# Performance work log

Measured on AMD Instinct MI355X. Metric: run time of the kernel, lower is better.

## Reference

```python
import jax, jax.numpy as jnp
import numpy as np

Nknn = 10
Np = 20
N = 524288
DOWN, LEFT, RIGHT, UP, WIDTH = -5.0, -5.0, 5.0, 5.0, 1.0


def setup_inputs() -> dict:
    key = jax.random.key(0)
    ks = jax.random.split(key, 20)
    def p(k, shape, fan_in):
        return jax.random.normal(k, shape, jnp.float32) / jnp.sqrt(jnp.float32(fan_in))
    inp = {
        "t": jax.random.uniform(ks[0], (1,), jnp.float32),
        "y": jax.random.normal(ks[1], (N, 4 + 2 * Np), jnp.float32),
        # net1: Linear(4,8) -> ReLU -> Linear(8,2)
        "w1a": p(ks[2], (4, 8), 4),   "b1a": p(ks[3], (8,), 4),
        "w1b": p(ks[4], (8, 2), 8),   "b1b": p(ks[5], (2,), 8),
        # net2: Linear(1,16) -> ReLU -> Linear(16,8) -> ReLU -> Linear(8,1)
        "w2a": p(ks[6], (1, 16), 1),  "b2a": p(ks[7], (16,), 1),
        "w2b": p(ks[8], (16, 8), 16), "b2b": p(ks[9], (8,), 16),
        "w2c": p(ks[10], (8, 1), 8),  "b2c": p(ks[11], (1,), 8),
        # net3: same architecture as net2
        "w3a": p(ks[12], (1, 16), 1), "b3a": p(ks[13], (16,), 1),
        "w3b": p(ks[14], (16, 8), 16),"b3b": p(ks[15], (8,), 16),
        "w3c": p(ks[16], (8, 1), 8),  "b3c": p(ks[17], (1,), 8),
    }
    return inp


def _mlp3(x, wa, ba, wb, bb, wc, bc):
    # Linear -> ReLU -> Linear -> ReLU -> Linear, applied on last axis
    h = jax.nn.relu(x @ wa + ba)
    h = jax.nn.relu(h @ wb + bb)
    return h @ wc + bc


def reference(t, y, w1a, b1a, w1b, b1b, w2a, b2a, w2b, b2b, w2c, b2c,
              w3a, b3a, w3b, b3b, w3c, b3c):
    y = y.astype(jnp.float32)
    theX = y[:, 0:2]            # positions [N,2]
    theV = y[:, 2:4]            # velocities [N,2]
    ux = y[:, 4:4 + 2 * Nknn].reshape(-1, Nknn, 2)  # neighbor offsets [N,Nknn,2]

    dxdt = theV

    # goal-attraction term f1
    door = jnp.array([RIGHT + 0.6, 0.0], jnp.float32)
    diff = door - theX
    unit_e = diff / jnp.sqrt(jnp.sum(diff * diff, axis=1, keepdims=True))
    h = jax.nn.relu(jnp.concatenate([unit_e, theV], axis=1) @ w1a + b1a)
    f1 = h @ w1b + b1b          # [N,2]

    # wall-repulsion term f2; rows inside the door gap get rightdist=100
    x0 = theX[:, 0:1]
    x1 = theX[:, 1:2]
    rightdist = jnp.where((x1 < WIDTH) & (x1 > -WIDTH), 100.0, RIGHT - x0)
    wall_in = jnp.stack([x0 - LEFT, x1 - DOWN, UP - x1, rightdist], axis=1)  # [N,4,1]
    o = _mlp3(wall_in, w2a, b2a, w2b, bb=b2b, wc=w2c, bc=b2c) if False else _mlp3(wall_in, w2a, b2a, w2b, b2b, w2c, b2c)  # [N,4,1]
    # directions: [1,0], [0,1], [0,-1], [-1,0]
    f2 = jnp.concatenate([o[:, 0] - o[:, 3], o[:, 1] - o[:, 2]], axis=1)  # [N,2]

    # neighbor-repulsion term f3 (vectorized over Nknn)
    d = jnp.sqrt(jnp.sum(ux * ux, axis=2, keepdims=True))  # [N,Nknn,1]
    f3 = -jnp.sum(_mlp3(d, w3a, b3a, w3b, b3b, w3c, b3c) * ux / d, axis=1)  # [N,2]

    dvdt = (f1 + f2 + f3) / 80.0
    dudt = jnp.zeros((y.shape[0], 2 * Nknn), y.dtype)
    result = jnp.concatenate([dxdt, dvdt, dudt], axis=1)  # [N, 4 + 2*Nknn]

    # zero out agents that have exited (x > RIGHT)
    result = jnp.where((theX[:, 0] > RIGHT)[:, None], 0.0, result)
    return result
```

## Files before the change

### kernel.cpp

```cpp
#include <hip/hip_runtime.h>

#define NROW  524288
#define BLK   256
#define TPB   2
#define NKNN  10
#define YCOLS 44
#define OCOLS 24

#define TBL    128
#define T2_LO  (-2.0f)
#define T3_LO  (0.0f)
#define T_H    (1.0f / 8.0f)
#define T_INVH 8.0f
#define SROW   25

typedef float f32x4 __attribute__((ext_vector_type(4)));

__device__ __forceinline__ float mlp_scalar_g(float s,
    const float* __restrict__ wa, const float* __restrict__ ba,
    const float* __restrict__ wb, const float* __restrict__ bb,
    const float* __restrict__ wc, const float* __restrict__ bc) {
    float h[16];
#pragma unroll
    for (int j = 0; j < 16; ++j)
        h[j] = fmaxf(fmaf(s, wa[j], ba[j]), 0.0f);
    float g[8];
#pragma unroll
    for (int k = 0; k < 8; ++k) g[k] = bb[k];
#pragma unroll
    for (int j = 0; j < 16; ++j) {
        float hj = h[j];
#pragma unroll
        for (int k = 0; k < 8; ++k)
            g[k] = fmaf(hj, wb[j * 8 + k], g[k]);
    }
    float o = bc[0];
#pragma unroll
    for (int k = 0; k < 8; ++k)
        o = fmaf(fmaxf(g[k], 0.0f), wc[k], o);
    return o;
}

__device__ __forceinline__ float tbl_eval(const float* __restrict__ T, float s, float lo) {
    float u = (s - lo) * T_INVH;
    u = fminf(fmaxf(u, 0.0f), (float)TBL - 1.001f);
    int i = (int)u;
    float f = u - (float)i;
    float va = T[i];
    float vb = T[i + 1];
    return fmaf(f, vb - va, va);
}

__device__ __forceinline__ void load_tile(const f32x4* __restrict__ yb,
                                          int w, int lane, f32x4 ld[6]) {
#pragma unroll
    for (int i = 0; i < 6; ++i) {
        int j  = lane + i * 64;
        int rr = j / 6;
        int cc = j - rr * 6;
        ld[i]  = yb[(64 * w + rr) * 11 + cc];
    }
}

__device__ __forceinline__ void stage_tile(float* __restrict__ Sf,
                                           int w, int lane, const f32x4 ld[6]) {
#pragma unroll
    for (int i = 0; i < 6; ++i) {
        int j  = lane + i * 64;
        int rr = j / 6;
        int cc = j - rr * 6;
        int base = (64 * w + rr) * SROW + 4 * cc;
        Sf[base + 0] = ld[i].x;
        Sf[base + 1] = ld[i].y;
        Sf[base + 2] = ld[i].z;
        Sf[base + 3] = ld[i].w;
    }
}

__device__ __forceinline__ void compute_row(float* __restrict__ Sf, int t,
    const float* __restrict__ T2v, const float* __restrict__ T3v, float o100,
    const float* __restrict__ w1a, const float* __restrict__ b1a,
    const float* __restrict__ w1b, const float* __restrict__ b1b)
{
    float* R = Sf + t * SROW;
    float x0 = R[0], x1 = R[1], vx = R[2], vy = R[3];
    float us[2 * NKNN];
#pragma unroll
    for (int m = 0; m < 2 * NKNN; ++m)
        us[m] = R[4 + m];

    float dx = 5.6f - x0;
    float dy = 0.0f - x1;
    float inv = rsqrtf(fmaf(dx, dx, dy * dy));
    float in1[4] = { dx * inv, dy * inv, vx, vy };
    float h1[8];
#pragma unroll
    for (int j = 0; j < 8; ++j) {
        float s = b1a[j];
#pragma unroll
        for (int k = 0; k < 4; ++k)
            s = fmaf(in1[k], w1a[k * 8 + j], s);
        h1[j] = fmaxf(s, 0.0f);
    }
    float f1x = b1b[0];
    float f1y = b1b[1];
#pragma unroll
    for (int j = 0; j < 8; ++j) {
        f1x = fmaf(h1[j], w1b[j * 2 + 0], f1x);
        f1y = fmaf(h1[j], w1b[j * 2 + 1], f1y);
    }

    bool corridor = (x1 < 1.0f) && (x1 > -1.0f);
    float o0 = tbl_eval(T2v, x0 + 5.0f, T2_LO);
    float o1 = tbl_eval(T2v, x1 + 5.0f, T2_LO);
    float o2 = tbl_eval(T2v, 5.0f - x1, T2_LO);
    float o3 = corridor ? o100 : tbl_eval(T2v, 5.0f - x0, T2_LO);
    float f2x = o0 - o3;
    float f2y = o1 - o2;

    float f3x = 0.0f, f3y = 0.0f;
#pragma unroll
    for (int n = 0; n < NKNN; ++n) {
        float uxn = us[2 * n + 0];
        float uyn = us[2 * n + 1];
        float s2  = fmaf(uxn, uxn, uyn * uyn);
        float idn = rsqrtf(s2);
        float d   = s2 * idn;
        float m   = tbl_eval(T3v, d, T3_LO);
        float c   = m * idn;
        f3x = fmaf(-c, uxn, f3x);
        f3y = fmaf(-c, uyn, f3y);
    }

    bool dead = (x0 > 5.0f);
    const float k80 = 1.0f / 80.0f;
    R[0] = dead ? 0.0f : vx;
    R[1] = dead ? 0.0f : vy;
    R[2] = dead ? 0.0f : (f1x + f2x + f3x) * k80;
    R[3] = dead ? 0.0f : (f1y + f2y + f3y) * k80;
}

__device__ __forceinline__ void store_tile(f32x4* __restrict__ ob,
                                           const float* __restrict__ Sf,
                                           int w, int lane) {
#pragma unroll
    for (int i = 0; i < 6; ++i) {
        int j  = lane + i * 64;
        int rr = j / 6;
        int cc = j - rr * 6;
        f32x4 v = (f32x4)(0.0f);
        if (cc == 0) {
            const float* R = Sf + (64 * w + rr) * SROW;
            v.x = R[0]; v.y = R[1]; v.z = R[2]; v.w = R[3];
        }
        __builtin_nontemporal_store(v, &ob[384 * w + j]);
    }
}

__global__ __launch_bounds__(BLK) void odefunc_kernel(
    const float* __restrict__ y,
    const float* __restrict__ w1a, const float* __restrict__ b1a,
    const float* __restrict__ w1b, const float* __restrict__ b1b,
    const float* __restrict__ w2a, const float* __restrict__ b2a,
    const float* __restrict__ w2b, const float* __restrict__ b2b,
    const float* __restrict__ w2c, const float* __restrict__ b2c,
    const float* __restrict__ w3a, const float* __restrict__ b3a,
    const float* __restrict__ w3b, const float* __restrict__ b3b,
    const float* __restrict__ w3c, const float* __restrict__ b3c,
    float* __restrict__ out)
{
    __shared__ float Sf[BLK * SROW];
    __shared__ float T2v[TBL];
    __shared__ float T3v[TBL];
    __shared__ float o100s;

    const int t    = threadIdx.x;
    const int w    = t >> 6;
    const int lane = t & 63;

    const f32x4* yb0 = reinterpret_cast<const f32x4*>(y)
                     + (size_t)blockIdx.x * TPB * BLK * (YCOLS / 4);
    const f32x4* yb1 = yb0 + BLK * (YCOLS / 4);
    f32x4* ob0 = reinterpret_cast<f32x4*>(out)
               + (size_t)blockIdx.x * TPB * BLK * (OCOLS / 4);
    f32x4* ob1 = ob0 + BLK * (OCOLS / 4);

    f32x4 ld0[6];
    load_tile(yb0, w, lane, ld0);

    if (t < TBL) {
        T2v[t] = mlp_scalar_g(T2_LO + (float)t * T_H, w2a, b2a, w2b, b2b, w2c, b2c);
        if (t == 0)
            o100s = mlp_scalar_g(100.0f, w2a, b2a, w2b, b2b, w2c, b2c);
    } else {
        int i3 = t - TBL;
        T3v[i3] = mlp_scalar_g(T3_LO + (float)i3 * T_H, w3a, b3a, w3b, b3b, w3c, b3c);
    }

    __syncthreads();
    const float o100 = o100s;

    stage_tile(Sf, w, lane, ld0);
    __builtin_amdgcn_wave_barrier();

    f32x4 ld1[6];
    load_tile(yb1, w, lane, ld1);

    compute_row(Sf, t, T2v, T3v, o100, w1a, b1a, w1b, b1b);
    __builtin_amdgcn_wave_barrier();
    store_tile(ob0, Sf, w, lane);
    __builtin_amdgcn_wave_barrier();

    stage_tile(Sf, w, lane, ld1);
    __builtin_amdgcn_wave_barrier();

    compute_row(Sf, t, T2v, T3v, o100, w1a, b1a, w1b, b1b);
    __builtin_amdgcn_wave_barrier();
    store_tile(ob1, Sf, w, lane);
}

extern "C" void kernel_launch(void* const* d_in, const int* in_sizes, int n_in,
                              void* d_out, int out_size, void* d_ws, size_t ws_size,
                              hipStream_t stream) {
    int iy = 1;
    for (int i = 0; i < n_in; ++i) {
        if (in_sizes[i] == NROW * YCOLS) { iy = i; break; }
    }
    const float* y   = (const float*)d_in[iy];
    const float* w1a = (const float*)d_in[iy + 1];
    const float* b1a = (const float*)d_in[iy + 2];
    const float* w1b = (const float*)d_in[iy + 3];
    const float* b1b = (const float*)d_in[iy + 4];
    const float* w2a = (const float*)d_in[iy + 5];
    const float* b2a = (const float*)d_in[iy + 6];
    const float* w2b = (const float*)d_in[iy + 7];
    const float* b2b = (const float*)d_in[iy + 8];
    const float* w2c = (const float*)d_in[iy + 9];
    const float* b2c = (const float*)d_in[iy + 10];
    const float* w3a = (const float*)d_in[iy + 11];
    const float* b3a = (const float*)d_in[iy + 12];
    const float* w3b = (const float*)d_in[iy + 13];
    const float* b3b = (const float*)d_in[iy + 14];
    const float* w3c = (const float*)d_in[iy + 15];
    const float* b3c = (const float*)d_in[iy + 16];
    float* out = (float*)d_out;

    hipLaunchKernelGGL(odefunc_kernel, dim3(NROW / (BLK * TPB)), dim3(BLK), 0, stream,
                       y, w1a, b1a, w1b, b1b,
                       w2a, b2a, w2b, b2b, w2c, b2c,
                       w3a, b3a, w3b, b3b, w3c, b3c, out);
}
```

Measured before the change: 25.90 us.

## Process one tile per block and stage rows in two LDS halves

The kernel goes from two 256-row tiles per block to one, doubling the grid. Each row is now staged through LDS in two passes: columns 0-11 first, then columns 12-23, with the stride reduced from 25 to 13 floats. The goal is to shrink LDS per block to raise occupancy and to overlap the second-half staging with the f1/f2 compute. The cost is that every block rebuilds its lookup tables, so twice as many blocks repeat that setup work.

```diff
diff --git a/kernel.cpp b/kernel.cpp
--- a/kernel.cpp
+++ b/kernel.cpp
@@ -2,7 +2,6 @@
 
 #define NROW  524288
 #define BLK   256
-#define TPB   2
 #define NKNN  10
 #define YCOLS 44
 #define OCOLS 24
@@ -12,7 +11,7 @@
 #define T3_LO  (0.0f)
 #define T_H    (1.0f / 8.0f)
 #define T_INVH 8.0f
-#define SROW   25
+#define SROW   13
 
 typedef float f32x4 __attribute__((ext_vector_type(4)));
 
@@ -49,112 +48,6 @@
     float va = T[i];
     float vb = T[i + 1];
     return fmaf(f, vb - va, va);
-}
-
-__device__ __forceinline__ void load_tile(const f32x4* __restrict__ yb,
-                                          int w, int lane, f32x4 ld[6]) {
-#pragma unroll
-    for (int i = 0; i < 6; ++i) {
-        int j  = lane + i * 64;
-        int rr = j / 6;
-        int cc = j - rr * 6;
-        ld[i]  = yb[(64 * w + rr) * 11 + cc];
-    }
-}
-
-__device__ __forceinline__ void stage_tile(float* __restrict__ Sf,
-                                           int w, int lane, const f32x4 ld[6]) {
-#pragma unroll
-    for (int i = 0; i < 6; ++i) {
-        int j  = lane + i * 64;
-        int rr = j / 6;
-        int cc = j - rr * 6;
-        int base = (64 * w + rr) * SROW + 4 * cc;
-        Sf[base + 0] = ld[i].x;
-        Sf[base + 1] = ld[i].y;
-        Sf[base + 2] = ld[i].z;
-        Sf[base + 3] = ld[i].w;
-    }
-}
-
-__device__ __forceinline__ void compute_row(float* __restrict__ Sf, int t,
-    const float* __restrict__ T2v, const float* __restrict__ T3v, float o100,
-    const float* __restrict__ w1a, const float* __restrict__ b1a,
-    const float* __restrict__ w1b, const float* __restrict__ b1b)
-{
-    float* R = Sf + t * SROW;
-    float x0 = R[0], x1 = R[1], vx = R[2], vy = R[3];
-    float us[2 * NKNN];
-#pragma unroll
-    for (int m = 0; m < 2 * NKNN; ++m)
-        us[m] = R[4 + m];
-
-    float dx = 5.6f - x0;
-    float dy = 0.0f - x1;
-    float inv = rsqrtf(fmaf(dx, dx, dy * dy));
-    float in1[4] = { dx * inv, dy * inv, vx, vy };
-    float h1[8];
-#pragma unroll
-    for (int j = 0; j < 8; ++j) {
-        float s = b1a[j];
-#pragma unroll
-        for (int k = 0; k < 4; ++k)
-            s = fmaf(in1[k], w1a[k * 8 + j], s);
-        h1[j] = fmaxf(s, 0.0f);
-    }
-    float f1x = b1b[0];
-    float f1y = b1b[1];
-#pragma unroll
-    for (int j = 0; j < 8; ++j) {
-        f1x = fmaf(h1[j], w1b[j * 2 + 0], f1x);
-        f1y = fmaf(h1[j], w1b[j * 2 + 1], f1y);
-    }
-
-    bool corridor = (x1 < 1.0f) && (x1 > -1.0f);
-    float o0 = tbl_eval(T2v, x0 + 5.0f, T2_LO);
-    float o1 = tbl_eval(T2v, x1 + 5.0f, T2_LO);
-    float o2 = tbl_eval(T2v, 5.0f - x1, T2_LO);
-    float o3 = corridor ? o100 : tbl_eval(T2v, 5.0f - x0, T2_LO);
-    float f2x = o0 - o3;
-    float f2y = o1 - o2;
-
-    float f3x = 0.0f, f3y = 0.0f;
-#pragma unroll
-    for (int n = 0; n < NKNN; ++n) {
-        float uxn = us[2 * n + 0];
-        float uyn = us[2 * n + 1];
-        float s2  = fmaf(uxn, uxn, uyn * uyn);
-        float idn = rsqrtf(s2);
-        float d   = s2 * idn;
-        float m   = tbl_eval(T3v, d, T3_LO);
-        float c   = m * idn;
-        f3x = fmaf(-c, uxn, f3x);
-        f3y = fmaf(-c, uyn, f3y);
-    }
-
-    bool dead = (x0 > 5.0f);
-    const float k80 = 1.0f / 80.0f;
-    R[0] = dead ? 0.0f : vx;
-    R[1] = dead ? 0.0f : vy;
-    R[2] = dead ? 0.0f : (f1x + f2x + f3x) * k80;
-    R[3] = dead ? 0.0f : (f1y + f2y + f3y) * k80;
-}
-
-__device__ __forceinline__ void store_tile(f32x4* __restrict__ ob,
-                                           const float* __restrict__ Sf,
-                                           int w, int lane) {
-#pragma unroll
-    for (int i = 0; i < 6; ++i) {
-        int j  = lane + i * 64;
-        int rr = j / 6;
-        int cc = j - rr * 6;
-        f32x4 v = (f32x4)(0.0f);
-        if (cc == 0) {
-            const float* R = Sf + (64 * w + rr) * SROW;
-            v.x = R[0]; v.y = R[1]; v.z = R[2]; v.w = R[3];
-        }
-        __builtin_nontemporal_store(v, &ob[384 * w + j]);
-    }
 }
 
 __global__ __launch_bounds__(BLK) void odefunc_kernel(
@@ -178,15 +71,29 @@
     const int w    = t >> 6;
     const int lane = t & 63;
 
-    const f32x4* yb0 = reinterpret_cast<const f32x4*>(y)
-                     + (size_t)blockIdx.x * TPB * BLK * (YCOLS / 4);
-    const f32x4* yb1 = yb0 + BLK * (YCOLS / 4);
-    f32x4* ob0 = reinterpret_cast<f32x4*>(out)
-               + (size_t)blockIdx.x * TPB * BLK * (OCOLS / 4);
-    f32x4* ob1 = ob0 + BLK * (OCOLS / 4);
-
-    f32x4 ld0[6];
-    load_tile(yb0, w, lane, ld0);
+    const f32x4* yb = reinterpret_cast<const f32x4*>(y)
+                    + (size_t)blockIdx.x * BLK * (YCOLS / 4);
+    f32x4* ob = reinterpret_cast<f32x4*>(out)
+              + (size_t)blockIdx.x * BLK * (OCOLS / 4);
+
+    f32x4 ldA[3], ldB[3];
+    int rrA[3], ccA[3], rrB[3], ccB[3];
+#pragma unroll
+    for (int i = 0; i < 3; ++i) {
+        int j  = lane + i * 64;
+        int rr = j / 3;
+        int cc = j - rr * 3;
+        rrA[i] = rr; ccA[i] = cc;
+        ldA[i] = yb[(64 * w + rr) * 11 + cc];
+    }
+#pragma unroll
+    for (int i = 0; i < 3; ++i) {
+        int j  = lane + i * 64;
+        int rr = j / 3;
+        int cc = j - rr * 3;
+        rrB[i] = rr; ccB[i] = cc;
+        ldB[i] = yb[(64 * w + rr) * 11 + (cc + 3)];
+    }
 
     if (t < TBL) {
         T2v[t] = mlp_scalar_g(T2_LO + (float)t * T_H, w2a, b2a, w2b, b2b, w2c, b2c);
@@ -200,23 +107,114 @@
     __syncthreads();
     const float o100 = o100s;
 
-    stage_tile(Sf, w, lane, ld0);
-    __builtin_amdgcn_wave_barrier();
-
-    f32x4 ld1[6];
-    load_tile(yb1, w, lane, ld1);
-
-    compute_row(Sf, t, T2v, T3v, o100, w1a, b1a, w1b, b1b);
-    __builtin_amdgcn_wave_barrier();
-    store_tile(ob0, Sf, w, lane);
-    __builtin_amdgcn_wave_barrier();
-
-    stage_tile(Sf, w, lane, ld1);
-    __builtin_amdgcn_wave_barrier();
-
-    compute_row(Sf, t, T2v, T3v, o100, w1a, b1a, w1b, b1b);
-    __builtin_amdgcn_wave_barrier();
-    store_tile(ob1, Sf, w, lane);
+#pragma unroll
+    for (int i = 0; i < 3; ++i) {
+        int base = (64 * w + rrA[i]) * SROW + 4 * ccA[i];
+        Sf[base + 0] = ldA[i].x;
+        Sf[base + 1] = ldA[i].y;
+        Sf[base + 2] = ldA[i].z;
+        Sf[base + 3] = ldA[i].w;
+    }
+    __builtin_amdgcn_wave_barrier();
+
+    float* R = Sf + t * SROW;
+    float x0 = R[0], x1 = R[1], vx = R[2], vy = R[3];
+    float uA[8];
+#pragma unroll
+    for (int m = 0; m < 8; ++m) uA[m] = R[4 + m];
+    __builtin_amdgcn_wave_barrier();
+
+    float dxm = 5.6f - x0;
+    float dym = 0.0f - x1;
+    float inv = rsqrtf(fmaf(dxm, dxm, dym * dym));
+    float in1[4] = { dxm * inv, dym * inv, vx, vy };
+    float h1[8];
+#pragma unroll
+    for (int j = 0; j < 8; ++j) {
+        float s = b1a[j];
+#pragma unroll
+        for (int k = 0; k < 4; ++k)
+            s = fmaf(in1[k], w1a[k * 8 + j], s);
+        h1[j] = fmaxf(s, 0.0f);
+    }
+    float f1x = b1b[0];
+    float f1y = b1b[1];
+#pragma unroll
+    for (int j = 0; j < 8; ++j) {
+        f1x = fmaf(h1[j], w1b[j * 2 + 0], f1x);
+        f1y = fmaf(h1[j], w1b[j * 2 + 1], f1y);
+    }
+
+    bool corridor = (x1 < 1.0f) && (x1 > -1.0f);
+    float o0 = tbl_eval(T2v, x0 + 5.0f, T2_LO);
+    float o1 = tbl_eval(T2v, x1 + 5.0f, T2_LO);
+    float o2 = tbl_eval(T2v, 5.0f - x1, T2_LO);
+    float o3 = corridor ? o100 : tbl_eval(T2v, 5.0f - x0, T2_LO);
+    float f2x = o0 - o3;
+    float f2y = o1 - o2;
+
+    float f3x = 0.0f, f3y = 0.0f;
+#pragma unroll
+    for (int n = 0; n < 4; ++n) {
+        float uxn = uA[2 * n + 0];
+        float uyn = uA[2 * n + 1];
+        float s2  = fmaf(uxn, uxn, uyn * uyn);
+        float idn = rsqrtf(s2);
+        float d   = s2 * idn;
+        float m   = tbl_eval(T3v, d, T3_LO);
+        float c   = m * idn;
+        f3x = fmaf(-c, uxn, f3x);
+        f3y = fmaf(-c, uyn, f3y);
+    }
+
+#pragma unroll
+    for (int i = 0; i < 3; ++i) {
+        int base = (64 * w + rrB[i]) * SROW + 4 * ccB[i];
+        Sf[base + 0] = ldB[i].x;
+        Sf[base + 1] = ldB[i].y;
+        Sf[base + 2] = ldB[i].z;
+        Sf[base + 3] = ldB[i].w;
+    }
+    __builtin_amdgcn_wave_barrier();
+
+    float uB[12];
+#pragma unroll
+    for (int m = 0; m < 12; ++m) uB[m] = R[m];
+    __builtin_amdgcn_wave_barrier();
+
+#pragma unroll
+    for (int n = 0; n < 6; ++n) {
+        float uxn = uB[2 * n + 0];
+        float uyn = uB[2 * n + 1];
+        float s2  = fmaf(uxn, uxn, uyn * uyn);
+        float idn = rsqrtf(s2);
+        float d   = s2 * idn;
+        float m   = tbl_eval(T3v, d, T3_LO);
+        float c   = m * idn;
+        f3x = fmaf(-c, uxn, f3x);
+        f3y = fmaf(-c, uyn, f3y);
+    }
+
+    bool dead = (x0 > 5.0f);
+    const float k80 = 1.0f / 80.0f;
+    R[0] = dead ? 0.0f : vx;
+    R[1] = dead ? 0.0f : vy;
+    R[2] = dead ? 0.0f : (f1x + f2x + f3x) * k80;
+    R[3] = dead ? 0.0f : (f1y + f2y + f3y) * k80;
+    __builtin_amdgcn_wave_barrier();
+
+#pragma unroll
+    for (int i = 0; i < 6; ++i) {
+        int j  = lane + i * 64;
+        int rr = j / 6;
+        int cc = j - rr * 6;
+        f32x4 v = (f32x4)(0.0f);
+        if (cc == 0) {
+            const float* Rr = Sf + (64 * w + rr) * SROW;
+            v.x = Rr[0]; v.y = Rr[1]; v.z = Rr[2]; v.w = Rr[3];
+        }
+        __builtin_nontemporal_store(v, &ob[384 * w + j]);
+    }
 }
 
 extern "C" void kernel_launch(void* const* d_in, const int* in_sizes, int n_in,
@@ -245,7 +243,7 @@
     const float* b3c = (const float*)d_in[iy + 16];
     float* out = (float*)d_out;
 
-    hipLaunchKernelGGL(odefunc_kernel, dim3(NROW / (BLK * TPB)), dim3(BLK), 0, stream,
+    hipLaunchKernelGGL(odefunc_kernel, dim3(NROW / BLK), dim3(BLK), 0, stream,
                        y, w1a, b1a, w1b, b1b,
                        w2a, b2a, w2b, b2b, w2c, b2c,
                        w3a, b3a, w3b, b3b, w3c, b3c, out);
```

After: 27.79 us. 7.3% more time.
